# Kernel optimization log

Hardware: AMD Instinct MI355X
Metric: run time of the kernel (lower is better)

## Reference

```python
import jax, jax.numpy as jnp
import numpy as np

B, T, K = 8192, 256, 16
N_TRANS = 4  # 0: s2u, 1: u2s_n0, 2: u2s_n1_d2, 3: u2s_n1_dgt2  (DistanceCRF)


def setup_inputs() -> dict:
    key = jax.random.key(0)
    ks = jax.random.split(key, 8)
    emissions = jax.random.normal(ks[0], (B, T, K), dtype=jnp.float32)
    tags = jax.random.randint(ks[1], (B, T), 0, K, dtype=jnp.int32)
    who2who = jax.random.randint(ks[2], (B, T - 1), 0, 2, dtype=jnp.int32)
    init_count = jax.random.randint(ks[3], (B, T - 1), 0, 2, dtype=jnp.int32)
    distance = jax.random.randint(ks[4], (B, T - 1), 0, 2, dtype=jnp.int32)
    class_weights = jax.random.uniform(ks[5], (K,), dtype=jnp.float32, minval=0.5, maxval=2.0)
    trans_stack = jax.random.normal(ks[6], (N_TRANS, K, K), dtype=jnp.float32) * 0.1
    start_scores = jax.random.normal(ks[7], (K,), dtype=jnp.float32) * 0.1
    return {
        'emissions': emissions, 'tags': tags, 'who2who': who2who,
        'init_count': init_count, 'distance': distance,
        'class_weights': class_weights, 'trans_stack': trans_stack,
        'start_scores': start_scores,
    }


def _trans_index(who2who, init_count, distance):
    # Mirrors MultiTurnCRF._get_trans for variant='DistanceCRF':
    #   w==1 -> s2u; w==0 & init_count==0 -> u2s_n0;
    #   w==0 & init>0 & distance==0 -> u2s_n1_d2; else u2s_n1_dgt2
    return jnp.where(who2who == 1, 0,
           jnp.where(init_count == 0, 1,
           jnp.where(distance == 0, 2, 3)))


def _crf_seq(em, tags, tidx, class_weights, trans_stack, start_scores):
    # em: [T, K], tags: [T], tidx: [T-1]
    w = class_weights[tags]                               # [T]
    em_gold = jnp.take_along_axis(em, tags[:, None], axis=1)[:, 0]   # [T]
    tr_gold = trans_stack[tidx, tags[:-1], tags[1:]]      # [T-1]
    gold = w[0] * (start_scores[tags[0]] + em_gold[0]) \
           + jnp.sum(w[1:] * (tr_gold + em_gold[1:]))

    def step(alpha, xs):
        ti, e = xs
        tr = trans_stack[ti]                              # [K, K]
        alpha = jax.nn.logsumexp(alpha[:, None] + tr + e[None, :], axis=0)
        return alpha, None

    alpha0 = start_scores + em[0]
    alphaT, _ = jax.lax.scan(step, alpha0, (tidx, em[1:]))
    log_Z = jax.nn.logsumexp(alphaT)
    return gold, log_Z


def reference(emissions, tags, who2who, init_count, distance,
              class_weights, trans_stack, start_scores):
    tidx = _trans_index(who2who, init_count, distance)    # [B, T-1]
    gold, log_Z = jax.vmap(_crf_seq, in_axes=(0, 0, 0, None, None, None))(
        emissions, tags, tidx, class_weights, trans_stack, start_scores)
    return gold, log_Z
```

## Files before the change

kernel.cpp:

```cpp
#include <hip/hip_runtime.h>

#define T_LEN 256
#define B_TOT 8192
#define RSCALE 3.2734375f
#define L2E    1.44269504f
#define LN2    0.693147180559945f

typedef __attribute__((ext_vector_type(2))) _Float16 h2;

__device__ __forceinline__ h2 pkrtz(float lo, float hi) {
    return __builtin_bit_cast(h2, __builtin_amdgcn_cvt_pkrtz(lo, hi));
}
__device__ __forceinline__ float ror8f(float x) {
    int xi = __float_as_int(x);
    int r = __builtin_amdgcn_update_dpp(xi, xi, 0x128, 0xF, 0xF, false);
    return __int_as_float(r);
}
__device__ __forceinline__ h2 ror1h(h2 x) {
    int xi = __builtin_bit_cast(int, x);
    int r = __builtin_amdgcn_update_dpp(xi, xi, 0x121, 0xF, 0xF, false);
    return __builtin_bit_cast(h2, r);
}

__global__ __launch_bounds__(256) void pack_ctrl(
    const int* __restrict__ tags, const int* __restrict__ w2w,
    const int* __restrict__ ic,   const int* __restrict__ ds,
    const float* __restrict__ cw, const float* __restrict__ trans,
    const float* __restrict__ start,
    unsigned char* __restrict__ ctrl, float* __restrict__ goldp)
{
    int idx = blockIdx.x * 256 + threadIdx.x;
    int b = idx >> 8, t = idx & 255;
    int tag = tags[idx];
    unsigned char byte = (unsigned char)tag;
    float g;
    if (t == 0) {
        g = cw[tag] * start[tag];
    } else {
        int off = b * (T_LEN - 1) + (t - 1);
        int tidx = (w2w[off] == 1) ? 0 : ((ic[off] == 0) ? 1 : ((ds[off] == 0) ? 2 : 3));
        byte |= (unsigned char)(tidx << 4);
        g = cw[tag] * trans[tidx * 256 + tags[idx - 1] * 16 + tag];
    }
    ctrl[idx]  = byte;
    goldp[idx] = g;
}

__global__ __launch_bounds__(256, 2) void crf_rec(
    const float* __restrict__ em, const float* __restrict__ trans,
    const float* __restrict__ start, const float* __restrict__ cw,
    const unsigned char* __restrict__ ctrl,
    float* __restrict__ gev, float* __restrict__ out)
{
    __shared__ float tl[1024];
    for (int i = threadIdx.x; i < 1024; i += 256) tl[i] = trans[i];
    __syncthreads();

    const int j   = threadIdx.x & 15;
    const int seq = (blockIdx.x * 256 + threadIdx.x) >> 4;

    int pr    = __builtin_amdgcn_update_dpp(j, j, 0x121, 0xF, 0xF, false);
    int delta = (pr - j) & 15;

    h2 D[4][8];
#pragma unroll
    for (int c = 0; c < 4; ++c)
#pragma unroll
        for (int r = 0; r < 8; ++r) {
            float lo = __expf(tl[c * 256 + ((j + r * delta) & 15) * 16 + j]);
            float hi = __expf(tl[c * 256 + ((j + (r + 8) * delta) & 15) * 16 + j]);
            D[c][r] = pkrtz(lo, hi);
        }

    const float cw_j = cw[j];
    const float st_j = start[j];
    const float* ep  = em + (size_t)seq * 4096 + j;
    const uint4* cp  = (const uint4*)(ctrl + (size_t)seq * 256);

    float emr[16];
#pragma unroll
    for (int k = 0; k < 16; ++k) emr[k] = ep[k * 16];
    uint4 cq = cp[0], cqn = cp[1];

    float u, ge, logC = 5.545177444479562f;
    {
        int tag0 = (int)(cq.x & 15u);
        u  = __expf(st_j + emr[0]) * 0.00390625f;
        ge = (j == tag0) ? cw_j * emr[0] : 0.0f;
        emr[0] = ep[16 * 16];
    }

    auto STEP = [&](int t, int k, bool pf) __attribute__((always_inline)) {
        unsigned dw = (k < 4) ? cq.x : (k < 8) ? cq.y : (k < 12) ? cq.z : cq.w;
        int sh = 8 * (k & 3);
        int tag   = (int)((dw >> sh) & 15u);
        bool modd = ((dw >> (sh + 4)) & 1u) != 0u;
        bool mhi  = ((dw >> (sh + 5)) & 1u) != 0u;

        float uh = ror8f(u);
        h2 P = pkrtz(u, uh);
        float s = 0.0f;
#pragma unroll
        for (int r = 0; r < 8; ++r) {
            if (r) P = ror1h(P);
            h2 e01 = modd ? D[1][r] : D[0][r];
            h2 e23 = modd ? D[3][r] : D[2][r];
            h2 e   = mhi ? e23 : e01;
            s = __builtin_amdgcn_fdot2(P, e, s, false);
        }
        float exf = __builtin_exp2f(fmaf(emr[k], L2E, -RSCALE * L2E));
        if (j == tag) ge = fmaf(cw_j, emr[k], ge);
        u = s * exf;
        if (pf) emr[k] = ep[(size_t)(t + 16) * 16];
        if ((k & 7) == 7) {
            float mx = u;
            mx = fmaxf(mx, __shfl_xor(mx, 1, 64));
            mx = fmaxf(mx, __shfl_xor(mx, 2, 64));
            mx = fmaxf(mx, __shfl_xor(mx, 4, 64));
            mx = fmaxf(mx, __shfl_xor(mx, 8, 64));
            int e2; (void)frexpf(mx, &e2);
            u = ldexpf(u, -e2 - 4);
            logC += (float)(e2 + 4) * LN2;
        }
    };

#pragma unroll
    for (int k = 1; k < 16; ++k) STEP(k, k, true);
    for (int blk = 1; blk < 15; ++blk) {
        cq = cqn;
        cqn = cp[blk + 1];
#pragma unroll
        for (int k = 0; k < 16; ++k) STEP(blk * 16 + k, k, true);
    }
    cq = cqn;
#pragma unroll
    for (int k = 0; k < 16; ++k) STEP(240 + k, k, false);

    float su = u, gs = ge;
#pragma unroll
    for (int m = 1; m < 16; m <<= 1) {
        su += __shfl_xor(su, m, 64);
        gs += __shfl_xor(gs, m, 64);
    }
    if (j == 0) {
        gev[seq] = gs;
        out[B_TOT + seq] = logf(su) + 255.0f * RSCALE + logC;
    }
}

__global__ __launch_bounds__(256) void gold_red(
    const float* __restrict__ goldp, const float* __restrict__ gev,
    float* __restrict__ out)
{
    int b = blockIdx.x * 4 + (threadIdx.x >> 6);
    int l = threadIdx.x & 63;
    const float* p = goldp + (size_t)b * 256;
    float s = (p[l] + p[l + 64]) + (p[l + 128] + p[l + 192]);
#pragma unroll
    for (int m = 1; m < 64; m <<= 1) s += __shfl_xor(s, m, 64);
    if (l == 0) out[b] = s + gev[b];
}

extern "C" void kernel_launch(void* const* d_in, const int* in_sizes, int n_in,
                              void* d_out, int out_size, void* d_ws, size_t ws_size,
                              hipStream_t stream) {
    const float* emissions     = (const float*)d_in[0];
    const int*   tags          = (const int*)  d_in[1];
    const int*   who2who       = (const int*)  d_in[2];
    const int*   init_count    = (const int*)  d_in[3];
    const int*   distance      = (const int*)  d_in[4];
    const float* class_weights = (const float*)d_in[5];
    const float* trans_stack   = (const float*)d_in[6];
    const float* start_scores  = (const float*)d_in[7];
    float* out = (float*)d_out;

    char* ws = (char*)d_ws;
    unsigned char* ctrl  = (unsigned char*)ws;
    float* goldp = (float*)(ws + (2 << 20));
    float* gev   = (float*)(ws + (10 << 20));

    hipLaunchKernelGGL(pack_ctrl, dim3(B_TOT), dim3(256), 0, stream,
                       tags, who2who, init_count, distance,
                       class_weights, trans_stack, start_scores, ctrl, goldp);

    hipLaunchKernelGGL(crf_rec, dim3(B_TOT * 16 / 256), dim3(256), 0, stream,
                       emissions, trans_stack, start_scores, class_weights,
                       ctrl, gev, out);

    hipLaunchKernelGGL(gold_red, dim3(B_TOT / 4), dim3(256), 0, stream,
                       goldp, gev, out);
}
```

Measured before the change: 251.6 us.

## Fuse control packing and gold reduction into the CRF recurrence kernel

```diff
diff --git a/kernel.cpp b/kernel.cpp
--- a/kernel.cpp
+++ b/kernel.cpp
@@ -22,42 +22,53 @@
     return __builtin_bit_cast(h2, r);
 }
 
-__global__ __launch_bounds__(256) void pack_ctrl(
+__global__ __launch_bounds__(256, 2) void crf_fused(
+    const float* __restrict__ em, const float* __restrict__ trans,
+    const float* __restrict__ start, const float* __restrict__ cw,
     const int* __restrict__ tags, const int* __restrict__ w2w,
     const int* __restrict__ ic,   const int* __restrict__ ds,
-    const float* __restrict__ cw, const float* __restrict__ trans,
-    const float* __restrict__ start,
-    unsigned char* __restrict__ ctrl, float* __restrict__ goldp)
-{
-    int idx = blockIdx.x * 256 + threadIdx.x;
-    int b = idx >> 8, t = idx & 255;
-    int tag = tags[idx];
-    unsigned char byte = (unsigned char)tag;
-    float g;
-    if (t == 0) {
-        g = cw[tag] * start[tag];
-    } else {
-        int off = b * (T_LEN - 1) + (t - 1);
-        int tidx = (w2w[off] == 1) ? 0 : ((ic[off] == 0) ? 1 : ((ds[off] == 0) ? 2 : 3));
-        byte |= (unsigned char)(tidx << 4);
-        g = cw[tag] * trans[tidx * 256 + tags[idx - 1] * 16 + tag];
-    }
-    ctrl[idx]  = byte;
-    goldp[idx] = g;
-}
-
-__global__ __launch_bounds__(256, 2) void crf_rec(
-    const float* __restrict__ em, const float* __restrict__ trans,
-    const float* __restrict__ start, const float* __restrict__ cw,
-    const unsigned char* __restrict__ ctrl,
-    float* __restrict__ gev, float* __restrict__ out)
+    float* __restrict__ out)
 {
     __shared__ float tl[1024];
-    for (int i = threadIdx.x; i < 1024; i += 256) tl[i] = trans[i];
+    __shared__ float cw_l[16];
+    __shared__ float st_l[16];
+    __shared__ uint4 ctrl4[256];
+    __shared__ float gl[4096];
+
+    const int tid = threadIdx.x;
+    for (int i = tid; i < 1024; i += 256) tl[i] = trans[i];
+    if (tid < 16)      cw_l[tid]      = cw[tid];
+    else if (tid < 32) st_l[tid - 16] = start[tid - 16];
     __syncthreads();
 
-    const int j   = threadIdx.x & 15;
-    const int seq = (blockIdx.x * 256 + threadIdx.x) >> 4;
+    {
+        unsigned char* ctrl_lds = (unsigned char*)ctrl4;
+        const int s0 = blockIdx.x * 16;
+        const int t  = tid;
+#pragma unroll 4
+        for (int m = 0; m < 16; ++m) {
+            int idx = (s0 + m) * 256 + t;
+            int tag = tags[idx];
+            unsigned byte = (unsigned)tag;
+            float g;
+            if (t == 0) {
+                g = cw_l[tag] * st_l[tag];
+            } else {
+                int off  = (s0 + m) * 255 + (t - 1);
+                int tidx = (w2w[off] == 1) ? 0 : ((ic[off] == 0) ? 1 : ((ds[off] == 0) ? 2 : 3));
+                byte |= (unsigned)(tidx << 4);
+                int ptag = tags[idx - 1];
+                g = cw_l[tag] * tl[tidx * 256 + ptag * 16 + tag];
+            }
+            ctrl_lds[m * 256 + t] = (unsigned char)byte;
+            gl[m * 256 + t] = g;
+        }
+    }
+    __syncthreads();
+
+    const int j   = tid & 15;
+    const int grp = tid >> 4;
+    const int seq = blockIdx.x * 16 + grp;
 
     int pr    = __builtin_amdgcn_update_dpp(j, j, 0x121, 0xF, 0xF, false);
     int delta = (pr - j) & 15;
@@ -72,10 +83,10 @@
             D[c][r] = pkrtz(lo, hi);
         }
 
-    const float cw_j = cw[j];
-    const float st_j = start[j];
+    const float cw_j = cw_l[j];
+    const float st_j = st_l[j];
     const float* ep  = em + (size_t)seq * 4096 + j;
-    const uint4* cp  = (const uint4*)(ctrl + (size_t)seq * 256);
+    const uint4* cp  = ctrl4 + grp * 16;
 
     float emr[16];
 #pragma unroll
@@ -136,29 +147,20 @@
 #pragma unroll
     for (int k = 0; k < 16; ++k) STEP(240 + k, k, false);
 
-    float su = u, gs = ge;
+    float gp = 0.0f;
+#pragma unroll
+    for (int q = 0; q < 16; ++q) gp += gl[grp * 256 + j + 16 * q];
+
+    float su = u, gs = ge + gp;
 #pragma unroll
     for (int m = 1; m < 16; m <<= 1) {
         su += __shfl_xor(su, m, 64);
         gs += __shfl_xor(gs, m, 64);
     }
     if (j == 0) {
-        gev[seq] = gs;
+        out[seq]         = gs;
         out[B_TOT + seq] = logf(su) + 255.0f * RSCALE + logC;
     }
-}
-
-__global__ __launch_bounds__(256) void gold_red(
-    const float* __restrict__ goldp, const float* __restrict__ gev,
-    float* __restrict__ out)
-{
-    int b = blockIdx.x * 4 + (threadIdx.x >> 6);
-    int l = threadIdx.x & 63;
-    const float* p = goldp + (size_t)b * 256;
-    float s = (p[l] + p[l + 64]) + (p[l + 128] + p[l + 192]);
-#pragma unroll
-    for (int m = 1; m < 64; m <<= 1) s += __shfl_xor(s, m, 64);
-    if (l == 0) out[b] = s + gev[b];
 }
 
 extern "C" void kernel_launch(void* const* d_in, const int* in_sizes, int n_in,
@@ -173,20 +175,9 @@
     const float* trans_stack   = (const float*)d_in[6];
     const float* start_scores  = (const float*)d_in[7];
     float* out = (float*)d_out;
+    (void)d_ws; (void)ws_size;
 
-    char* ws = (char*)d_ws;
-    unsigned char* ctrl  = (unsigned char*)ws;
-    float* goldp = (float*)(ws + (2 << 20));
-    float* gev   = (float*)(ws + (10 << 20));
-
-    hipLaunchKernelGGL(pack_ctrl, dim3(B_TOT), dim3(256), 0, stream,
-                       tags, who2who, init_count, distance,
-                       class_weights, trans_stack, start_scores, ctrl, goldp);
-
-    hipLaunchKernelGGL(crf_rec, dim3(B_TOT * 16 / 256), dim3(256), 0, stream,
+    hipLaunchKernelGGL(crf_fused, dim3(B_TOT / 16), dim3(256), 0, stream,
                        emissions, trans_stack, start_scores, class_weights,
-                       ctrl, gev, out);
-
-    hipLaunchKernelGGL(gold_red, dim3(B_TOT / 4), dim3(256), 0, stream,
-                       goldp, gev, out);
+                       tags, who2who, init_count, distance, out);
 }
```

New measurement: 266.7 us. +6.0%, slower.
